# Kernel optimization log

Measured on AMD Instinct MI355X. Metric: run time of the kernel, lower is better.

The kernel has to match this reference:

```python
import jax, jax.numpy as jnp
import numpy as np

B, T, I, H = 4096, 512, 3, 64


def setup_inputs() -> dict:
    key = jax.random.key(0)
    ks = jax.random.split(key, 8)
    s = 1.0 / np.sqrt(H)  # PyTorch LSTM init scale
    x = jax.random.normal(ks[0], (B, T, I), dtype=jnp.float32)
    W_ih = jax.random.uniform(ks[1], (4 * H, I), minval=-s, maxval=s, dtype=jnp.float32)
    W_hh = jax.random.uniform(ks[2], (4 * H, H), minval=-s, maxval=s, dtype=jnp.float32)
    b_ih = jax.random.uniform(ks[3], (4 * H,), minval=-s, maxval=s, dtype=jnp.float32)
    b_hh = jax.random.uniform(ks[4], (4 * H,), minval=-s, maxval=s, dtype=jnp.float32)
    W_dec = jax.random.uniform(ks[5], (I, H), minval=-s, maxval=s, dtype=jnp.float32)
    b_dec = jax.random.uniform(ks[6], (I,), minval=-s, maxval=s, dtype=jnp.float32)
    return {"x": x, "W_ih": W_ih, "W_hh": W_hh, "b_ih": b_ih, "b_hh": b_hh,
            "W_dec": W_dec, "b_dec": b_dec}


def _lstm(x, W_ih, W_hh, b_ih, b_hh):
    # Precompute input contribution for all timesteps: [B, T, 4H]
    x_gates = jnp.einsum('bti,gi->btg', x, W_ih) + b_ih + b_hh
    h0 = jnp.zeros((x.shape[0], H), dtype=x.dtype)
    c0 = jnp.zeros((x.shape[0], H), dtype=x.dtype)

    def step(carry, xg_t):
        h, c = carry
        gates = xg_t + h @ W_hh.T  # [B, 4H]
        i_g, f_g, g_g, o_g = jnp.split(gates, 4, axis=-1)  # PyTorch order i,f,g,o
        i_g = jax.nn.sigmoid(i_g)
        f_g = jax.nn.sigmoid(f_g)
        g_g = jnp.tanh(g_g)
        o_g = jax.nn.sigmoid(o_g)
        c_new = f_g * c + i_g * g_g
        h_new = o_g * jnp.tanh(c_new)
        return (h_new, c_new), h_new

    _, hs = jax.lax.scan(step, (h0, c0), jnp.swapaxes(x_gates, 0, 1))  # [T, B, H]
    return jnp.swapaxes(hs, 0, 1)  # [B, T, H]


def reference(x, W_ih, W_hh, b_ih, b_hh, W_dec, b_dec):
    lstm_out = _lstm(x, W_ih, W_hh, b_ih, b_hh)
    return jnp.einsum('bth,oh->bto', lstm_out, W_dec) + b_dec  # [B, T, I]
```

## Files before the change

### kernel.cpp

```cpp
#include <hip/hip_runtime.h>


#define TLEN 512
#define TCHUNK 64

typedef float  float4_t __attribute__((ext_vector_type(4)));
typedef __bf16 bf16x8   __attribute__((ext_vector_type(8)));
typedef unsigned int uint2_t __attribute__((ext_vector_type(2)));

__device__ __forceinline__ float fexp2(float x){ return __builtin_amdgcn_exp2f(x); }
__device__ __forceinline__ float frcp (float x){ return __builtin_amdgcn_rcpf(x); }
__device__ __forceinline__ float sigm (float x){ return frcp(1.f + fexp2(-1.44269504f*x)); }
__device__ __forceinline__ float tanh_(float x){ return 1.f - 2.f*frcp(1.f + fexp2(2.88539008f*x)); }

__device__ __forceinline__ void split8(const float* v, bf16x8& hi, bf16x8& lo){
  #pragma unroll
  for (int j = 0; j < 8; j++){
    __bf16 h = (__bf16)v[j];
    hi[j] = h;
    lo[j] = (__bf16)(v[j] - (float)h);
  }
}

#define MFMA(a,b,c) __builtin_amdgcn_mfma_f32_16x16x32_bf16((a),(b),(c),0,0,0)

#define HHI 0
#define HLO 2304
#define XPH 4608
#define XPL 8704
#define HS_SZ 12800
#define XOF 0
#define OOF 3136
#define LF_SZ 6272

__global__ __launch_bounds__(256, 1)
void LSTMAnomalyDetector_kernel(
    const float* __restrict__ x,     const float* __restrict__ W_ih,
    const float* __restrict__ W_hh,  const float* __restrict__ b_ih,
    const float* __restrict__ b_hh,  const float* __restrict__ W_dec,
    const float* __restrict__ b_dec, float* __restrict__ out)
{
  __shared__ __align__(16) unsigned short HS[HS_SZ];
  __shared__ __align__(16) float          LF[LF_SZ];

  const int tid  = threadIdx.x;
  const int w    = tid >> 6;
  const int lane = tid & 63;
  const int q    = lane >> 4;
  const int lid  = lane & 15;
  const int b0   = blockIdx.x * 16;
  const int cw   = w*16 + lid;

  bf16x8 Bh[4][2], Bl[4][2];
  bf16x8 Xh[4],    Xl[4];
  bf16x8 Dh[2],    Dl[2];

  #pragma unroll
  for (int tl = 0; tl < 4; tl++){
    const int g = tl*64 + cw;
    #pragma unroll
    for (int kt = 0; kt < 2; kt++){
      const float* p = W_hh + g*64 + kt*32 + q*8;
      float v[8];
      #pragma unroll
      for (int j = 0; j < 8; j++) v[j] = p[j];
      split8(v, Bh[tl][kt], Bl[tl][kt]);
    }
    float v[8] = {0.f,0.f,0.f,0.f,0.f,0.f,0.f,0.f};
    if (q == 0){
      v[0] = W_ih[g*3+0]; v[1] = W_ih[g*3+1]; v[2] = W_ih[g*3+2];
      v[3] = b_ih[g] + b_hh[g];
    }
    split8(v, Xh[tl], Xl[tl]);
  }
  #pragma unroll
  for (int kt = 0; kt < 2; kt++){
    float v[8] = {0.f,0.f,0.f,0.f,0.f,0.f,0.f,0.f};
    if (lid < 3){
      const float* p = W_dec + lid*64 + kt*32 + q*8;
      #pragma unroll
      for (int j = 0; j < 8; j++) v[j] = p[j];
    }
    split8(v, Dh[kt], Dl[kt]);
  }
  const float bdec = (lid < 3) ? b_dec[lid] : 0.f;

  bf16x8 ah[2] = {}, al[2] = {};
  float creg[4] = {0.f, 0.f, 0.f, 0.f};

  #pragma unroll
  for (int s = 0; s < 3; s++){
    const int f = tid + 256*s; const int row = f/48; const int off = (f%48)*4;
    float4_t v = *(const float4_t*)(x + (size_t)(b0+row)*1536 + off);
    *(float4_t*)&LF[XOF + row*196 + off] = v;
  }
  __syncthreads();
  #pragma unroll
  for (int s = 0; s < 4; s++){
    const int p = tid + 256*s;
    const float* xp = &LF[XOF + (p & 15)*196 + (p >> 4)*3];
    const unsigned u0 = __float_as_uint(xp[0]);
    const unsigned u1 = __float_as_uint(xp[1]);
    const unsigned u2 = __float_as_uint(xp[2]);
    const float l0 = xp[0] - __uint_as_float(u0 & 0xFFFF0000u);
    const float l1 = xp[1] - __uint_as_float(u1 & 0xFFFF0000u);
    const float l2 = xp[2] - __uint_as_float(u2 & 0xFFFF0000u);
    uint2_t hi, lo;
    hi[0] = (u0 >> 16) | (u1 & 0xFFFF0000u);
    hi[1] = (u2 >> 16) | 0x3F800000u;
    lo[0] = (__float_as_uint(l0) >> 16) | (__float_as_uint(l1) & 0xFFFF0000u);
    lo[1] = (__float_as_uint(l2) >> 16);
    *(uint2_t*)&HS[XPH + p*4] = hi;
    *(uint2_t*)&HS[XPL + p*4] = lo;
  }
  __syncthreads();

  for (int t = 0; t < TLEN; ++t){
    const int dt = t & (TCHUNK-1);
    const int hb = (t & 1) * 1152;

    uint2_t xh2 = *(const uint2_t*)&HS[XPH + (dt*16 + lid)*4];
    uint2_t xl2 = *(const uint2_t*)&HS[XPL + (dt*16 + lid)*4];
    xh2 = (q == 0) ? xh2 : (uint2_t)0;
    xl2 = (q == 0) ? xl2 : (uint2_t)0;
    union U8 { unsigned u[4]; bf16x8 v; };
    U8 uxh; uxh.u[0]=xh2[0]; uxh.u[1]=xh2[1]; uxh.u[2]=0u; uxh.u[3]=0u;
    U8 uxl; uxl.u[0]=xl2[0]; uxl.u[1]=xl2[1]; uxl.u[2]=0u; uxl.u[3]=0u;
    const bf16x8 xah = uxh.v, xal = uxl.v;

    float4_t g4[4];
    #pragma unroll
    for (int tl = 0; tl < 4; tl++){
      float4_t accA = {0.f,0.f,0.f,0.f};
      float4_t accB = {0.f,0.f,0.f,0.f};
      accA = MFMA(ah[0], Bh[tl][0], accA);
      accA = MFMA(ah[1], Bh[tl][1], accA);
      accA = MFMA(al[0], Bh[tl][0], accA);
      accA = MFMA(al[1], Bh[tl][1], accA);
      accB = MFMA(ah[0], Bl[tl][0], accB);
      accB = MFMA(ah[1], Bl[tl][1], accB);
      accB = MFMA(xah,   Xh[tl],    accB);
      accB = MFMA(xal,   Xh[tl],    accB);
      accB = MFMA(xah,   Xl[tl],    accB);
      g4[tl] = accA + accB;
    }

    #pragma unroll
    for (int r = 0; r < 4; r++){
      const float ig = sigm (g4[0][r]);
      const float fg = sigm (g4[1][r]);
      const float gg = tanh_(g4[2][r]);
      const float og = sigm (g4[3][r]);
      creg[r] = fg*creg[r] + ig*gg;
      const float h = og * tanh_(creg[r]);
      const unsigned u  = __float_as_uint(h);
      const float    lf = h - __uint_as_float(u & 0xFFFF0000u);
      const int m = q*4 + r;
      HS[HHI + hb + m*72 + cw] = (unsigned short)(u >> 16);
      HS[HLO + hb + m*72 + cw] = (unsigned short)(__float_as_uint(lf) >> 16);
    }
    __syncthreads();

    {
      const unsigned short* ph = &HS[HHI + hb + lid*72 + q*8];
      const unsigned short* pl = &HS[HLO + hb + lid*72 + q*8];
      ah[0] = *(const bf16x8*)&ph[0];
      ah[1] = *(const bf16x8*)&ph[32];
      al[0] = *(const bf16x8*)&pl[0];
      al[1] = *(const bf16x8*)&pl[32];
    }

    if (w == 0){
      float4_t d = {0.f,0.f,0.f,0.f};
      d = MFMA(ah[0], Dh[0], d);
      d = MFMA(ah[1], Dh[1], d);
      d = MFMA(al[0], Dh[0], d);
      d = MFMA(al[1], Dh[1], d);
      d = MFMA(ah[0], Dl[0], d);
      d = MFMA(ah[1], Dl[1], d);
      if (lid < 3){
        #pragma unroll
        for (int r = 0; r < 4; r++)
          LF[OOF + (q*4+r)*196 + dt*3 + lid] = d[r] + bdec;
      }
    }

    if (dt == TCHUNK-1){
      __syncthreads();
      const int t0 = t - (TCHUNK-1);
      #pragma unroll
      for (int s = 0; s < 3; s++){
        const int f = tid + 256*s; const int row = f/48; const int off = (f%48)*4;
        float4_t v = *(const float4_t*)&LF[OOF + row*196 + off];
        *(float4_t*)(out + (size_t)(b0+row)*1536 + t0*3 + off) = v;
      }
      if (t + 1 < TLEN){
        #pragma unroll
        for (int s = 0; s < 3; s++){
          const int f = tid + 256*s; const int row = f/48; const int off = (f%48)*4;
          float4_t v = *(const float4_t*)(x + (size_t)(b0+row)*1536 + (t+1)*3 + off);
          *(float4_t*)&LF[XOF + row*196 + off] = v;
        }
        __syncthreads();
        #pragma unroll
        for (int s = 0; s < 4; s++){
          const int p = tid + 256*s;
          const float* xp = &LF[XOF + (p & 15)*196 + (p >> 4)*3];
          const unsigned u0 = __float_as_uint(xp[0]);
          const unsigned u1 = __float_as_uint(xp[1]);
          const unsigned u2 = __float_as_uint(xp[2]);
          const float l0 = xp[0] - __uint_as_float(u0 & 0xFFFF0000u);
          const float l1 = xp[1] - __uint_as_float(u1 & 0xFFFF0000u);
          const float l2 = xp[2] - __uint_as_float(u2 & 0xFFFF0000u);
          uint2_t hi, lo;
          hi[0] = (u0 >> 16) | (u1 & 0xFFFF0000u);
          hi[1] = (u2 >> 16) | 0x3F800000u;
          lo[0] = (__float_as_uint(l0) >> 16) | (__float_as_uint(l1) & 0xFFFF0000u);
          lo[1] = (__float_as_uint(l2) >> 16);
          *(uint2_t*)&HS[XPH + p*4] = hi;
          *(uint2_t*)&HS[XPL + p*4] = lo;
        }
      }
      __syncthreads();
    }
  }
}

extern "C" void kernel_launch(void* const* d_in, const int* in_sizes, int n_in,
                              void* d_out, int out_size, void* d_ws, size_t ws_size,
                              hipStream_t stream)
{
  const float* x     = (const float*)d_in[0];
  const float* W_ih  = (const float*)d_in[1];
  const float* W_hh  = (const float*)d_in[2];
  const float* b_ih  = (const float*)d_in[3];
  const float* b_hh  = (const float*)d_in[4];
  const float* W_dec = (const float*)d_in[5];
  const float* b_dec = (const float*)d_in[6];
  float* out = (float*)d_out;

  const int B = in_sizes[0] / (TLEN * 3);
  const int blocks = B / 16;
  hipLaunchKernelGGL(LSTMAnomalyDetector_kernel, dim3(blocks), dim3(256), 0, stream,
                     x, W_ih, W_hh, b_ih, b_hh, W_dec, b_dec, out);
}
```

Measured before the change: 529.8 us.

## Compute input gate projection in FP32 FMAs instead of split-bf16 MFMAs

The input projection x·W_ih + bias is now computed with scalar FP32 FMAs and used as the MFMA accumulator's initial value. This drops three MFMAs per gate tile per step and the bf16 hi/lo packing of x. The next step's input gates are computed ahead, between the recurrent MFMAs and the activations, so that work can hide under MFMA latency. The decoder MFMA now rotates across the four waves, and the decoder bias is folded into the accumulator init. The cost is extra VGPRs for the W_ih and bias values and the prefetched gate values.

After: 545.1 us. +2.9%, slower.

```diff
diff --git a/kernel.cpp b/kernel.cpp
--- a/kernel.cpp
+++ b/kernel.cpp
@@ -6,7 +6,6 @@
 
 typedef float  float4_t __attribute__((ext_vector_type(4)));
 typedef __bf16 bf16x8   __attribute__((ext_vector_type(8)));
-typedef unsigned int uint2_t __attribute__((ext_vector_type(2)));
 
 __device__ __forceinline__ float fexp2(float x){ return __builtin_amdgcn_exp2f(x); }
 __device__ __forceinline__ float frcp (float x){ return __builtin_amdgcn_rcpf(x); }
@@ -26,12 +25,11 @@
 
 #define HHI 0
 #define HLO 2304
-#define XPH 4608
-#define XPL 8704
-#define HS_SZ 12800
+#define HS_SZ 4608
 #define XOF 0
 #define OOF 3136
-#define LF_SZ 6272
+#define XP4 6272
+#define LF_SZ 10368
 
 __global__ __launch_bounds__(256, 1)
 void LSTMAnomalyDetector_kernel(
@@ -52,8 +50,8 @@
   const int cw   = w*16 + lid;
 
   bf16x8 Bh[4][2], Bl[4][2];
-  bf16x8 Xh[4],    Xl[4];
   bf16x8 Dh[2],    Dl[2];
+  float  Wi0[4], Wi1[4], Wi2[4], bia[4];
 
   #pragma unroll
   for (int tl = 0; tl < 4; tl++){
@@ -66,12 +64,10 @@
       for (int j = 0; j < 8; j++) v[j] = p[j];
       split8(v, Bh[tl][kt], Bl[tl][kt]);
     }
-    float v[8] = {0.f,0.f,0.f,0.f,0.f,0.f,0.f,0.f};
-    if (q == 0){
-      v[0] = W_ih[g*3+0]; v[1] = W_ih[g*3+1]; v[2] = W_ih[g*3+2];
-      v[3] = b_ih[g] + b_hh[g];
-    }
-    split8(v, Xh[tl], Xl[tl]);
+    Wi0[tl] = W_ih[g*3+0];
+    Wi1[tl] = W_ih[g*3+1];
+    Wi2[tl] = W_ih[g*3+2];
+    bia[tl] = b_ih[g] + b_hh[g];
   }
   #pragma unroll
   for (int kt = 0; kt < 2; kt++){
@@ -87,6 +83,7 @@
 
   bf16x8 ah[2] = {}, al[2] = {};
   float creg[4] = {0.f, 0.f, 0.f, 0.f};
+  float4_t xg[4];
 
   #pragma unroll
   for (int s = 0; s < 3; s++){
@@ -99,50 +96,48 @@
   for (int s = 0; s < 4; s++){
     const int p = tid + 256*s;
     const float* xp = &LF[XOF + (p & 15)*196 + (p >> 4)*3];
-    const unsigned u0 = __float_as_uint(xp[0]);
-    const unsigned u1 = __float_as_uint(xp[1]);
-    const unsigned u2 = __float_as_uint(xp[2]);
-    const float l0 = xp[0] - __uint_as_float(u0 & 0xFFFF0000u);
-    const float l1 = xp[1] - __uint_as_float(u1 & 0xFFFF0000u);
-    const float l2 = xp[2] - __uint_as_float(u2 & 0xFFFF0000u);
-    uint2_t hi, lo;
-    hi[0] = (u0 >> 16) | (u1 & 0xFFFF0000u);
-    hi[1] = (u2 >> 16) | 0x3F800000u;
-    lo[0] = (__float_as_uint(l0) >> 16) | (__float_as_uint(l1) & 0xFFFF0000u);
-    lo[1] = (__float_as_uint(l2) >> 16);
-    *(uint2_t*)&HS[XPH + p*4] = hi;
-    *(uint2_t*)&HS[XPL + p*4] = lo;
+    float4_t v = {xp[0], xp[1], xp[2], 0.f};
+    *(float4_t*)&LF[XP4 + p*4] = v;
   }
   __syncthreads();
+  #pragma unroll
+  for (int r = 0; r < 4; r++){
+    const float4_t xv = *(const float4_t*)&LF[XP4 + (q*4+r)*4];
+    #pragma unroll
+    for (int tl = 0; tl < 4; tl++)
+      xg[tl][r] = __builtin_fmaf(xv[0], Wi0[tl],
+                  __builtin_fmaf(xv[1], Wi1[tl],
+                  __builtin_fmaf(xv[2], Wi2[tl], bia[tl])));
+  }
 
   for (int t = 0; t < TLEN; ++t){
     const int dt = t & (TCHUNK-1);
     const int hb = (t & 1) * 1152;
 
-    uint2_t xh2 = *(const uint2_t*)&HS[XPH + (dt*16 + lid)*4];
-    uint2_t xl2 = *(const uint2_t*)&HS[XPL + (dt*16 + lid)*4];
-    xh2 = (q == 0) ? xh2 : (uint2_t)0;
-    xl2 = (q == 0) ? xl2 : (uint2_t)0;
-    union U8 { unsigned u[4]; bf16x8 v; };
-    U8 uxh; uxh.u[0]=xh2[0]; uxh.u[1]=xh2[1]; uxh.u[2]=0u; uxh.u[3]=0u;
-    U8 uxl; uxl.u[0]=xl2[0]; uxl.u[1]=xl2[1]; uxl.u[2]=0u; uxl.u[3]=0u;
-    const bf16x8 xah = uxh.v, xal = uxl.v;
-
     float4_t g4[4];
     #pragma unroll
     for (int tl = 0; tl < 4; tl++){
-      float4_t accA = {0.f,0.f,0.f,0.f};
-      float4_t accB = {0.f,0.f,0.f,0.f};
-      accA = MFMA(ah[0], Bh[tl][0], accA);
-      accA = MFMA(ah[1], Bh[tl][1], accA);
-      accA = MFMA(al[0], Bh[tl][0], accA);
-      accA = MFMA(al[1], Bh[tl][1], accA);
-      accB = MFMA(ah[0], Bl[tl][0], accB);
-      accB = MFMA(ah[1], Bl[tl][1], accB);
-      accB = MFMA(xah,   Xh[tl],    accB);
-      accB = MFMA(xal,   Xh[tl],    accB);
-      accB = MFMA(xah,   Xl[tl],    accB);
-      g4[tl] = accA + accB;
+      float4_t a = xg[tl];
+      a = MFMA(ah[0], Bh[tl][0], a);
+      a = MFMA(ah[1], Bh[tl][1], a);
+      a = MFMA(al[0], Bh[tl][0], a);
+      a = MFMA(al[1], Bh[tl][1], a);
+      a = MFMA(ah[0], Bl[tl][0], a);
+      a = MFMA(ah[1], Bl[tl][1], a);
+      g4[tl] = a;
+    }
+
+    float4_t nxg[4];
+    if (dt != TCHUNK-1){
+      #pragma unroll
+      for (int r = 0; r < 4; r++){
+        const float4_t xv = *(const float4_t*)&LF[XP4 + ((dt+1)*16 + q*4+r)*4];
+        #pragma unroll
+        for (int tl = 0; tl < 4; tl++)
+          nxg[tl][r] = __builtin_fmaf(xv[0], Wi0[tl],
+                       __builtin_fmaf(xv[1], Wi1[tl],
+                       __builtin_fmaf(xv[2], Wi2[tl], bia[tl])));
+      }
     }
 
     #pragma unroll
@@ -170,8 +165,8 @@
       al[1] = *(const bf16x8*)&pl[32];
     }
 
-    if (w == 0){
-      float4_t d = {0.f,0.f,0.f,0.f};
+    if (w == (t & 3)){
+      float4_t d = {bdec, bdec, bdec, bdec};
       d = MFMA(ah[0], Dh[0], d);
       d = MFMA(ah[1], Dh[1], d);
       d = MFMA(al[0], Dh[0], d);
@@ -181,7 +176,7 @@
       if (lid < 3){
         #pragma unroll
         for (int r = 0; r < 4; r++)
-          LF[OOF + (q*4+r)*196 + dt*3 + lid] = d[r] + bdec;
+          LF[OOF + (q*4+r)*196 + dt*3 + lid] = d[r];
       }
     }
 
@@ -206,23 +201,24 @@
         for (int s = 0; s < 4; s++){
           const int p = tid + 256*s;
           const float* xp = &LF[XOF + (p & 15)*196 + (p >> 4)*3];
-          const unsigned u0 = __float_as_uint(xp[0]);
-          const unsigned u1 = __float_as_uint(xp[1]);
-          const unsigned u2 = __float_as_uint(xp[2]);
-          const float l0 = xp[0] - __uint_as_float(u0 & 0xFFFF0000u);
-          const float l1 = xp[1] - __uint_as_float(u1 & 0xFFFF0000u);
-          const float l2 = xp[2] - __uint_as_float(u2 & 0xFFFF0000u);
-          uint2_t hi, lo;
-          hi[0] = (u0 >> 16) | (u1 & 0xFFFF0000u);
-          hi[1] = (u2 >> 16) | 0x3F800000u;
-          lo[0] = (__float_as_uint(l0) >> 16) | (__float_as_uint(l1) & 0xFFFF0000u);
-          lo[1] = (__float_as_uint(l2) >> 16);
-          *(uint2_t*)&HS[XPH + p*4] = hi;
-          *(uint2_t*)&HS[XPL + p*4] = lo;
+          float4_t v = {xp[0], xp[1], xp[2], 0.f};
+          *(float4_t*)&LF[XP4 + p*4] = v;
         }
-      }
-      __syncthreads();
-    }
+        __syncthreads();
+        #pragma unroll
+        for (int r = 0; r < 4; r++){
+          const float4_t xv = *(const float4_t*)&LF[XP4 + (q*4+r)*4];
+          #pragma unroll
+          for (int tl = 0; tl < 4; tl++)
+            nxg[tl][r] = __builtin_fmaf(xv[0], Wi0[tl],
+                         __builtin_fmaf(xv[1], Wi1[tl],
+                         __builtin_fmaf(xv[2], Wi2[tl], bia[tl])));
+        }
+      }
+    }
+
+    #pragma unroll
+    for (int tl = 0; tl < 4; tl++) xg[tl] = nxg[tl];
   }
 }
 
```
